# Kernel optimization log

Hardware: AMD Instinct MI355X
Metric: run time of the kernel (lower is better)

Reference implementation:

```python
import jax, jax.numpy as jnp
import numpy as np

NUM_SLOTS = 2048
LATENT_DIM = 512
EPS = 1e-12  # torch F.normalize clamps norm at eps


def _l2_normalize(x, axis):
    n = jnp.linalg.norm(x, axis=axis, keepdims=True)
    return x / jnp.maximum(n, EPS)


def setup_inputs() -> dict:
    key = jax.random.key(0)
    k_z, k_m = jax.random.split(key)
    z = jax.random.normal(k_z, (65536, LATENT_DIM), dtype=jnp.float32)
    memory = jax.random.normal(k_m, (NUM_SLOTS, LATENT_DIM), dtype=jnp.float32)
    return {"z": z, "memory": memory}


def reference(z, memory):
    # cosine-similarity attention over memory slots
    z_norm = _l2_normalize(z, axis=1)          # [B, D]
    mem_norm = _l2_normalize(memory, axis=1)   # [N, D]
    attn = jax.nn.softmax(z_norm @ mem_norm.T, axis=1)  # [B, N]
    z_hat = attn @ memory                      # [B, D] (unnormalized memory, as in source)
    return (z_hat, attn)
```

## Files before the change

kernel.cpp:

```cpp
#include <hip/hip_runtime.h>

#define NSLOTS 2048
#define DIM    512

typedef __bf16 bf16x8 __attribute__((ext_vector_type(8)));
typedef float  f32x4  __attribute__((ext_vector_type(4)));
typedef unsigned short us4 __attribute__((ext_vector_type(4)));
typedef unsigned short us8 __attribute__((ext_vector_type(8)));

typedef const __attribute__((address_space(1))) unsigned* gp_t;
typedef __attribute__((address_space(3))) unsigned* sp_t;

__device__ __forceinline__ void gl16(const void* g, void* l) {
    __builtin_amdgcn_global_load_lds((gp_t)g, (sp_t)l, 16, 0, 0);
}

__device__ __forceinline__ unsigned short f2bf(float f) {
    unsigned u = __builtin_bit_cast(unsigned, f);
    u = (u + 0x7FFFu + ((u >> 16) & 1u)) >> 16;
    return (unsigned short)u;
}
__device__ __forceinline__ float bf2f(unsigned short u) {
    unsigned v = ((unsigned)u) << 16;
    return __builtin_bit_cast(float, v);
}

__global__ __launch_bounds__(512) void prep_kernel(const float* __restrict__ mem,
                                                   unsigned short* __restrict__ memN,
                                                   unsigned short* __restrict__ memT) {
    __shared__ unsigned short T[32][516];
    const int tid = threadIdx.x;
    const int sl  = tid >> 4;
    const int c16 = tid & 15;
    const int n   = blockIdx.x * 32 + sl;
    const f32x4* row = (const f32x4*)(mem + (size_t)n * DIM);
    f32x4 v[8];
    float s = 0.f;
    #pragma unroll
    for (int j = 0; j < 8; ++j) {
        v[j] = row[c16*8 + j];
        s += v[j][0]*v[j][0] + v[j][1]*v[j][1] + v[j][2]*v[j][2] + v[j][3]*v[j][3];
    }
    #pragma unroll
    for (int off = 1; off < 16; off <<= 1) s += __shfl_xor(s, off);
    const float rn = 1.0f / fmaxf(sqrtf(s), 1e-12f);
    #pragma unroll
    for (int j = 0; j < 8; ++j) {
        us4 p, q;
        #pragma unroll
        for (int e = 0; e < 4; ++e) { p[e] = f2bf(v[j][e] * rn); q[e] = f2bf(v[j][e]); }
        *(us4*)(memN + (size_t)n * DIM + c16*32 + j*4) = p;
        *(us4*)(&T[sl][c16*32 + j*4]) = q;
    }
    __syncthreads();
    {
        const int d = tid;
        const int c4 = tid & 3;
        #pragma unroll
        for (int i = 0; i < 4; ++i) {
            const int dd = i*128 + (tid >> 2);
            us8 g;
            #pragma unroll
            for (int j = 0; j < 8; ++j) g[j] = T[c4*8 + j][dd];
            *(us8*)(memT + (size_t)dd * NSLOTS + blockIdx.x*32 + c4*8) = g;
        }
        (void)d;
    }
}

__global__ __launch_bounds__(512) void zprep_kernel(const float* __restrict__ z,
                                                    float* attnB) {
    const int tid = threadIdx.x;
    const size_t row = (size_t)blockIdx.x * 64 + (tid >> 3);
    const int c8 = tid & 7;
    const f32x4* zr = (const f32x4*)(z + row * DIM);
    f32x4 v[16];
    float s = 0.f;
    #pragma unroll
    for (int j = 0; j < 16; ++j) {
        v[j] = __builtin_nontemporal_load(zr + c8 + j*8);
        s += v[j][0]*v[j][0] + v[j][1]*v[j][1] + v[j][2]*v[j][2] + v[j][3]*v[j][3];
    }
    s += __shfl_xor(s, 1); s += __shfl_xor(s, 2); s += __shfl_xor(s, 4);
    const float rn = 1.0f / fmaxf(sqrtf(s), 1e-12f);
    char* dst = (char*)attnB + row * 8192 + 3072;
    #pragma unroll
    for (int j = 0; j < 16; ++j) {
        us4 p;
        #pragma unroll
        for (int e = 0; e < 4; ++e) p[e] = f2bf(v[j][e] * rn);
        *(us4*)(dst + c8*8 + j*64) = p;
    }
}

__global__ __launch_bounds__(512, 4) void k1_kernel(const unsigned short* __restrict__ memN,
                                                    float* attnB,
                                                    float* __restrict__ sums) {
    __shared__ char sb[2][24576];
    __shared__ float wsums[4][64];
    const int tid  = threadIdx.x;
    const int wid  = tid >> 6;
    const int lane = tid & 63;
    const int l16  = lane & 15;
    const int l4   = lane >> 4;
    const int m    = wid >> 2, n = wid & 3;
    const size_t rowbase = (size_t)blockIdx.x * 64;
    const char* attnRd = (const char*)attnB;

    auto stage = [&](int buf, int t) {
        const int c = t >> 3, ks = t & 7;
        {
            const int f = wid*64 + lane, ar = f >> 3, g = f & 7;
            const char* src = attnRd + (rowbase + ar) * 8192 + 3072 + ks*128
                            + ((g*16) ^ ((ar & 7) << 4));
            gl16(src, &sb[buf][0] + wid*1024);
        }
        #pragma unroll
        for (int i = 0; i < 2; ++i) {
            const int f = (i*8 + wid)*64 + lane, br = f >> 3, g = f & 7;
            const char* src = (const char*)memN + (size_t)(c*128 + br) * 1024 + ks*128
                            + ((g*16) ^ ((br & 7) << 4));
            gl16(src, &sb[buf][8192] + (i*8 + wid)*1024);
        }
    };

    const f32x4 zeroV = {0.f, 0.f, 0.f, 0.f};
    f32x4 acc[2][2];
    #pragma unroll
    for (int mt = 0; mt < 2; ++mt)
        #pragma unroll
        for (int nt = 0; nt < 2; ++nt) acc[mt][nt] = zeroV;
    float psum[2][4];
    #pragma unroll
    for (int mt = 0; mt < 2; ++mt)
        #pragma unroll
        for (int r = 0; r < 4; ++r) psum[mt][r] = 0.f;

    stage(0, 0);
    __syncthreads();

    for (int t = 0; t < 128; ++t) {
        const int c = t >> 3, ks = t & 7;
        if (t < 127) stage((t + 1) & 1, t + 1);
        const char* Ab = (const char*)&sb[t & 1][0];
        const char* Bb = (const char*)&sb[t & 1][8192];
        #pragma unroll
        for (int kk = 0; kk < 2; ++kk) {
            bf16x8 af[2];
            #pragma unroll
            for (int mt = 0; mt < 2; ++mt) {
                const int ar = m*32 + mt*16 + l16;
                af[mt] = *(const bf16x8*)(Ab + ar*128 + ((kk*64 + l4*16) ^ ((ar & 7) << 4)));
            }
            #pragma unroll
            for (int nt = 0; nt < 2; ++nt) {
                const int br = n*32 + nt*16 + l16;
                bf16x8 b = *(const bf16x8*)(Bb + br*128 + ((kk*64 + l4*16) ^ ((br & 7) << 4)));
                acc[0][nt] = __builtin_amdgcn_mfma_f32_16x16x32_bf16(af[0], b, acc[0][nt], 0, 0, 0);
                acc[1][nt] = __builtin_amdgcn_mfma_f32_16x16x32_bf16(af[1], b, acc[1][nt], 0, 0, 0);
            }
        }
        __syncthreads();
        if (ks == 7) {
            char* Pl = (char*)&sb[t & 1][0];
            #pragma unroll
            for (int mt = 0; mt < 2; ++mt)
                #pragma unroll
                for (int nt = 0; nt < 2; ++nt)
                    #pragma unroll
                    for (int r = 0; r < 4; ++r) {
                        const float e = __expf(acc[mt][nt][r]);
                        psum[mt][r] += e;
                        const int row = m*32 + mt*16 + l4*4 + r;
                        const int sl  = n*32 + nt*16 + l16;
                        *(unsigned short*)(Pl + row*256 + (((sl >> 3) * 16) ^ ((row & 7) << 4)) + (sl & 7)*2) = f2bf(e);
                        acc[mt][nt][r] = 0.f;
                    }
            __syncthreads();
            {
                const int prow = tid >> 3;
                #pragma unroll
                for (int h = 0; h < 2; ++h) {
                    const int g = (tid & 7) + h*8;
                    us8 pv = *(const us8*)(Pl + prow*256 + ((g*16) ^ ((prow & 7) << 4)));
                    __builtin_nontemporal_store(pv,
                        (us8*)((char*)attnB + (rowbase + prow) * 8192 + 4096 + c*256 + g*16));
                }
            }
            __syncthreads();
        }
    }

    #pragma unroll
    for (int mt = 0; mt < 2; ++mt)
        #pragma unroll
        for (int r = 0; r < 4; ++r) {
            #pragma unroll
            for (int off = 1; off < 16; off <<= 1) psum[mt][r] += __shfl_xor(psum[mt][r], off);
        }
    if (l16 == 0) {
        #pragma unroll
        for (int mt = 0; mt < 2; ++mt)
            #pragma unroll
            for (int r = 0; r < 4; ++r)
                wsums[n][m*32 + mt*16 + l4*4 + r] = psum[mt][r];
    }
    __syncthreads();
    if (tid < 64) sums[rowbase + tid] = wsums[0][tid] + wsums[1][tid] + wsums[2][tid] + wsums[3][tid];
}

__global__ __launch_bounds__(512, 4) void k2_kernel(const unsigned short* __restrict__ memT,
                                                    const float* __restrict__ sums,
                                                    float* __restrict__ zhat,
                                                    float* attnB) {
    __shared__ char ab[2][8192];
    __shared__ char bb[2][16384];
    __shared__ float rsums[64];
    const int tid  = threadIdx.x;
    const int wid  = tid >> 6;
    const int lane = tid & 63;
    const int l16  = lane & 15;
    const int l4   = lane >> 4;
    const int m    = wid >> 2, n = wid & 3;
    const size_t rowbase = (size_t)blockIdx.x * 64;
    const char* attnRd = (const char*)attnB;

    auto stageA = [&](int buf, int ks) {
        const int f = wid*64 + lane, ar = f >> 3, g = f & 7;
        const char* src = attnRd + (rowbase + ar) * 8192 + 4096 + ks*128
                        + ((g*16) ^ ((ar & 7) << 4));
        gl16(src, &ab[buf][0] + wid*1024);
    };
    auto stageB = [&](int buf, int ks, int nb) {
        #pragma unroll
        for (int i = 0; i < 2; ++i) {
            const int f = (i*8 + wid)*64 + lane, dr = f >> 3, g = f & 7;
            const char* src = (const char*)memT + (size_t)(nb*128 + dr) * 4096 + ks*128
                            + ((g*16) ^ ((dr & 7) << 4));
            gl16(src, &bb[buf][0] + (i*8 + wid)*1024);
        }
    };

    if (tid < 64) rsums[tid] = 1.0f / sums[rowbase + tid];

    const f32x4 zeroV = {0.f, 0.f, 0.f, 0.f};
    f32x4 acc[4][2][2];
    #pragma unroll
    for (int nb = 0; nb < 4; ++nb)
        #pragma unroll
        for (int mt = 0; mt < 2; ++mt)
            #pragma unroll
            for (int nt = 0; nt < 2; ++nt) acc[nb][mt][nt] = zeroV;

    stageA(0, 0);
    stageB(0, 0, 0);
    __syncthreads();

    for (int ks = 0; ks < 32; ++ks) {
        #pragma unroll
        for (int nb = 0; nb < 4; ++nb) {
            const int u = ks*4 + nb;
            if (nb < 3) stageB((u + 1) & 1, ks, nb + 1);
            else if (ks < 31) { stageA((ks + 1) & 1, ks + 1); stageB((u + 1) & 1, ks + 1, 0); }
            const char* Ab = (const char*)&ab[ks & 1][0];
            const char* Bb = (const char*)&bb[u & 1][0];
            if (nb == 0) {
                const int prow = tid >> 3;
                const int g = tid & 7;
                const float sc = rsums[prow];
                us8 pv = *(const us8*)(Ab + prow*128 + ((g*16) ^ ((prow & 7) << 4)));
                f32x4 o0, o1;
                #pragma unroll
                for (int e = 0; e < 4; ++e) { o0[e] = bf2f(pv[e]) * sc; o1[e] = bf2f(pv[e + 4]) * sc; }
                float* dst = attnB + (rowbase + prow) * NSLOTS + ks*64 + g*8;
                __builtin_nontemporal_store(o0, (f32x4*)dst);
                __builtin_nontemporal_store(o1, (f32x4*)(dst + 4));
            }
            #pragma unroll
            for (int kk = 0; kk < 2; ++kk) {
                bf16x8 af[2];
                #pragma unroll
                for (int mt = 0; mt < 2; ++mt) {
                    const int ar = m*32 + mt*16 + l16;
                    af[mt] = *(const bf16x8*)(Ab + ar*128 + ((kk*64 + l4*16) ^ ((ar & 7) << 4)));
                }
                #pragma unroll
                for (int nt = 0; nt < 2; ++nt) {
                    const int dr = n*32 + nt*16 + l16;
                    bf16x8 b = *(const bf16x8*)(Bb + dr*128 + ((kk*64 + l4*16) ^ ((dr & 7) << 4)));
                    acc[nb][0][nt] = __builtin_amdgcn_mfma_f32_16x16x32_bf16(af[0], b, acc[nb][0][nt], 0, 0, 0);
                    acc[nb][1][nt] = __builtin_amdgcn_mfma_f32_16x16x32_bf16(af[1], b, acc[nb][1][nt], 0, 0, 0);
                }
            }
            __syncthreads();
        }
    }

    #pragma unroll
    for (int nb = 0; nb < 4; ++nb)
        #pragma unroll
        for (int mt = 0; mt < 2; ++mt)
            #pragma unroll
            for (int r = 0; r < 4; ++r) {
                const int row = m*32 + mt*16 + l4*4 + r;
                const float rs = rsums[row];
                float* zr = zhat + (rowbase + row) * DIM + nb*128 + n*32 + l16;
                __builtin_nontemporal_store(acc[nb][mt][0][r] * rs, zr);
                __builtin_nontemporal_store(acc[nb][mt][1][r] * rs, zr + 16);
            }
}

extern "C" void kernel_launch(void* const* d_in, const int* in_sizes, int n_in,
                              void* d_out, int out_size, void* d_ws, size_t ws_size,
                              hipStream_t stream) {
    const float* zin = (const float*)d_in[0];
    const float* mem = (const float*)d_in[1];
    const int B = in_sizes[0] / DIM;
    unsigned short* memN = (unsigned short*)d_ws;
    unsigned short* memT = memN + (size_t)NSLOTS * DIM;
    float* sums = (float*)(memT + (size_t)NSLOTS * DIM);
    float* zhat = (float*)d_out;
    float* attn = zhat + (size_t)B * DIM;
    prep_kernel<<<NSLOTS / 32, 512, 0, stream>>>(mem, memN, memT);
    zprep_kernel<<<B / 64, 512, 0, stream>>>(zin, attn);
    k1_kernel<<<B / 64, 512, 0, stream>>>(memN, attn, sums);
    k2_kernel<<<B / 64, 512, 0, stream>>>(memT, sums, zhat, attn);
}
```

Baseline: 554.1 us.

## Fuse z normalization into k1, keep A resident in LDS, widen tiles

The separate zprep kernel is removed. k1 now normalizes z rows itself and keeps the full 64x512 bf16 A tile resident in LDS, so A no longer round-trips through global memory. k1's slot tile per chunk doubles to 256, and k2's K-step doubles to 256 bytes per row. In exchange, LDS use per block grows sharply (about 128KB in k1 and 96KB in k2) and the minimum-occupancy hint is dropped, which cuts the number of resident blocks per CU.

```diff
diff --git a/kernel.cpp b/kernel.cpp
--- a/kernel.cpp
+++ b/kernel.cpp
@@ -54,7 +54,6 @@
     }
     __syncthreads();
     {
-        const int d = tid;
         const int c4 = tid & 3;
         #pragma unroll
         for (int i = 0; i < 4; ++i) {
@@ -64,39 +63,15 @@
             for (int j = 0; j < 8; ++j) g[j] = T[c4*8 + j][dd];
             *(us8*)(memT + (size_t)dd * NSLOTS + blockIdx.x*32 + c4*8) = g;
         }
-        (void)d;
-    }
-}
-
-__global__ __launch_bounds__(512) void zprep_kernel(const float* __restrict__ z,
-                                                    float* attnB) {
-    const int tid = threadIdx.x;
-    const size_t row = (size_t)blockIdx.x * 64 + (tid >> 3);
-    const int c8 = tid & 7;
-    const f32x4* zr = (const f32x4*)(z + row * DIM);
-    f32x4 v[16];
-    float s = 0.f;
-    #pragma unroll
-    for (int j = 0; j < 16; ++j) {
-        v[j] = __builtin_nontemporal_load(zr + c8 + j*8);
-        s += v[j][0]*v[j][0] + v[j][1]*v[j][1] + v[j][2]*v[j][2] + v[j][3]*v[j][3];
-    }
-    s += __shfl_xor(s, 1); s += __shfl_xor(s, 2); s += __shfl_xor(s, 4);
-    const float rn = 1.0f / fmaxf(sqrtf(s), 1e-12f);
-    char* dst = (char*)attnB + row * 8192 + 3072;
-    #pragma unroll
-    for (int j = 0; j < 16; ++j) {
-        us4 p;
-        #pragma unroll
-        for (int e = 0; e < 4; ++e) p[e] = f2bf(v[j][e] * rn);
-        *(us4*)(dst + c8*8 + j*64) = p;
-    }
-}
-
-__global__ __launch_bounds__(512, 4) void k1_kernel(const unsigned short* __restrict__ memN,
-                                                    float* attnB,
-                                                    float* __restrict__ sums) {
-    __shared__ char sb[2][24576];
+    }
+}
+
+__global__ __launch_bounds__(512) void k1_kernel(const float* __restrict__ z,
+                                                 const unsigned short* __restrict__ memN,
+                                                 float* attnB,
+                                                 float* __restrict__ sums) {
+    __shared__ char As[65536];
+    __shared__ char Bs[2][32768];
     __shared__ float wsums[4][64];
     const int tid  = threadIdx.x;
     const int wid  = tid >> 6;
@@ -105,56 +80,70 @@
     const int l4   = lane >> 4;
     const int m    = wid >> 2, n = wid & 3;
     const size_t rowbase = (size_t)blockIdx.x * 64;
-    const char* attnRd = (const char*)attnB;
-
-    auto stage = [&](int buf, int t) {
+
+    {
+        const int r = tid >> 3, c8 = tid & 7;
+        const f32x4* zr = (const f32x4*)(z + (rowbase + r) * DIM);
+        f32x4 v[16];
+        float s = 0.f;
+        #pragma unroll
+        for (int j = 0; j < 16; ++j) {
+            v[j] = __builtin_nontemporal_load(zr + c8 + j*8);
+            s += v[j][0]*v[j][0] + v[j][1]*v[j][1] + v[j][2]*v[j][2] + v[j][3]*v[j][3];
+        }
+        s += __shfl_xor(s, 1); s += __shfl_xor(s, 2); s += __shfl_xor(s, 4);
+        const float rn = 1.0f / fmaxf(sqrtf(s), 1e-12f);
+        char* arow = As + r*1024;
+        #pragma unroll
+        for (int j = 0; j < 16; ++j) {
+            us4 p;
+            #pragma unroll
+            for (int e = 0; e < 4; ++e) p[e] = f2bf(v[j][e] * rn);
+            *(us4*)(arow + ((c8*8 + j*64) ^ ((r & 7) << 4))) = p;
+        }
+    }
+
+    auto stageB = [&](int buf, int t) {
         const int c = t >> 3, ks = t & 7;
-        {
-            const int f = wid*64 + lane, ar = f >> 3, g = f & 7;
-            const char* src = attnRd + (rowbase + ar) * 8192 + 3072 + ks*128
-                            + ((g*16) ^ ((ar & 7) << 4));
-            gl16(src, &sb[buf][0] + wid*1024);
-        }
-        #pragma unroll
-        for (int i = 0; i < 2; ++i) {
+        #pragma unroll
+        for (int i = 0; i < 4; ++i) {
             const int f = (i*8 + wid)*64 + lane, br = f >> 3, g = f & 7;
-            const char* src = (const char*)memN + (size_t)(c*128 + br) * 1024 + ks*128
+            const char* src = (const char*)memN + (size_t)(c*256 + br) * 1024 + ks*128
                             + ((g*16) ^ ((br & 7) << 4));
-            gl16(src, &sb[buf][8192] + (i*8 + wid)*1024);
+            gl16(src, &Bs[buf][(i*8 + wid)*1024]);
         }
     };
 
     const f32x4 zeroV = {0.f, 0.f, 0.f, 0.f};
-    f32x4 acc[2][2];
+    f32x4 acc[2][4];
     #pragma unroll
     for (int mt = 0; mt < 2; ++mt)
         #pragma unroll
-        for (int nt = 0; nt < 2; ++nt) acc[mt][nt] = zeroV;
+        for (int nt = 0; nt < 4; ++nt) acc[mt][nt] = zeroV;
     float psum[2][4];
     #pragma unroll
     for (int mt = 0; mt < 2; ++mt)
         #pragma unroll
         for (int r = 0; r < 4; ++r) psum[mt][r] = 0.f;
 
-    stage(0, 0);
+    stageB(0, 0);
     __syncthreads();
 
-    for (int t = 0; t < 128; ++t) {
+    for (int t = 0; t < 64; ++t) {
         const int c = t >> 3, ks = t & 7;
-        if (t < 127) stage((t + 1) & 1, t + 1);
-        const char* Ab = (const char*)&sb[t & 1][0];
-        const char* Bb = (const char*)&sb[t & 1][8192];
+        if (t < 63) stageB((t + 1) & 1, t + 1);
+        const char* Bb = (const char*)&Bs[t & 1][0];
         #pragma unroll
         for (int kk = 0; kk < 2; ++kk) {
             bf16x8 af[2];
             #pragma unroll
             for (int mt = 0; mt < 2; ++mt) {
                 const int ar = m*32 + mt*16 + l16;
-                af[mt] = *(const bf16x8*)(Ab + ar*128 + ((kk*64 + l4*16) ^ ((ar & 7) << 4)));
-            }
-            #pragma unroll
-            for (int nt = 0; nt < 2; ++nt) {
-                const int br = n*32 + nt*16 + l16;
+                af[mt] = *(const bf16x8*)(As + ar*1024 + ((ks*128 + kk*64 + l4*16) ^ ((ar & 7) << 4)));
+            }
+            #pragma unroll
+            for (int nt = 0; nt < 4; ++nt) {
+                const int br = n*64 + nt*16 + l16;
                 bf16x8 b = *(const bf16x8*)(Bb + br*128 + ((kk*64 + l4*16) ^ ((br & 7) << 4)));
                 acc[0][nt] = __builtin_amdgcn_mfma_f32_16x16x32_bf16(af[0], b, acc[0][nt], 0, 0, 0);
                 acc[1][nt] = __builtin_amdgcn_mfma_f32_16x16x32_bf16(af[1], b, acc[1][nt], 0, 0, 0);
@@ -162,29 +151,28 @@
         }
         __syncthreads();
         if (ks == 7) {
-            char* Pl = (char*)&sb[t & 1][0];
+            char* Pl = (char*)&Bs[t & 1][0];
             #pragma unroll
             for (int mt = 0; mt < 2; ++mt)
                 #pragma unroll
-                for (int nt = 0; nt < 2; ++nt)
+                for (int nt = 0; nt < 4; ++nt)
                     #pragma unroll
                     for (int r = 0; r < 4; ++r) {
                         const float e = __expf(acc[mt][nt][r]);
                         psum[mt][r] += e;
                         const int row = m*32 + mt*16 + l4*4 + r;
-                        const int sl  = n*32 + nt*16 + l16;
-                        *(unsigned short*)(Pl + row*256 + (((sl >> 3) * 16) ^ ((row & 7) << 4)) + (sl & 7)*2) = f2bf(e);
+                        const int sl  = n*64 + nt*16 + l16;
+                        *(unsigned short*)(Pl + row*512 + (((sl >> 3) * 16) ^ ((row & 7) << 4)) + (sl & 7)*2) = f2bf(e);
                         acc[mt][nt][r] = 0.f;
                     }
             __syncthreads();
             {
-                const int prow = tid >> 3;
-                #pragma unroll
-                for (int h = 0; h < 2; ++h) {
-                    const int g = (tid & 7) + h*8;
-                    us8 pv = *(const us8*)(Pl + prow*256 + ((g*16) ^ ((prow & 7) << 4)));
-                    __builtin_nontemporal_store(pv,
-                        (us8*)((char*)attnB + (rowbase + prow) * 8192 + 4096 + c*256 + g*16));
+                const int prow = tid >> 3, g8 = tid & 7;
+                char* gdst = (char*)attnB + (rowbase + prow) * 8192 + 4096 + c*512;
+                #pragma unroll
+                for (int h = 0; h < 4; ++h) {
+                    us8 pv = *(const us8*)(Pl + prow*512 + (((g8 + h*8)*16) ^ ((prow & 7) << 4)));
+                    __builtin_nontemporal_store(pv, (us8*)(gdst + (g8 + h*8)*16));
                 }
             }
             __syncthreads();
@@ -209,12 +197,12 @@
     if (tid < 64) sums[rowbase + tid] = wsums[0][tid] + wsums[1][tid] + wsums[2][tid] + wsums[3][tid];
 }
 
-__global__ __launch_bounds__(512, 4) void k2_kernel(const unsigned short* __restrict__ memT,
-                                                    const float* __restrict__ sums,
-                                                    float* __restrict__ zhat,
-                                                    float* attnB) {
-    __shared__ char ab[2][8192];
-    __shared__ char bb[2][16384];
+__global__ __launch_bounds__(512) void k2_kernel(const unsigned short* __restrict__ memT,
+                                                 const float* __restrict__ sums,
+                                                 float* __restrict__ zhat,
+                                                 float* attnB) {
+    __shared__ char ab[2][16384];
+    __shared__ char bb[2][32768];
     __shared__ float rsums[64];
     const int tid  = threadIdx.x;
     const int wid  = tid >> 6;
@@ -225,19 +213,22 @@
     const size_t rowbase = (size_t)blockIdx.x * 64;
     const char* attnRd = (const char*)attnB;
 
-    auto stageA = [&](int buf, int ks) {
-        const int f = wid*64 + lane, ar = f >> 3, g = f & 7;
-        const char* src = attnRd + (rowbase + ar) * 8192 + 4096 + ks*128
-                        + ((g*16) ^ ((ar & 7) << 4));
-        gl16(src, &ab[buf][0] + wid*1024);
+    auto stageA = [&](int buf, int ks2) {
+        #pragma unroll
+        for (int i = 0; i < 2; ++i) {
+            const int f = (i*8 + wid)*64 + lane, ar = f >> 4, g = f & 15;
+            const char* src = attnRd + (rowbase + ar) * 8192 + 4096 + ks2*256
+                            + ((g*16) ^ ((ar & 7) << 4));
+            gl16(src, &ab[buf][(i*8 + wid)*1024]);
+        }
     };
-    auto stageB = [&](int buf, int ks, int nb) {
-        #pragma unroll
-        for (int i = 0; i < 2; ++i) {
-            const int f = (i*8 + wid)*64 + lane, dr = f >> 3, g = f & 7;
-            const char* src = (const char*)memT + (size_t)(nb*128 + dr) * 4096 + ks*128
+    auto stageB = [&](int buf, int ks2, int nb) {
+        #pragma unroll
+        for (int i = 0; i < 4; ++i) {
+            const int f = (i*8 + wid)*64 + lane, dr = f >> 4, g = f & 15;
+            const char* src = (const char*)memT + (size_t)(nb*128 + dr) * 4096 + ks2*256
                             + ((g*16) ^ ((dr & 7) << 4));
-            gl16(src, &bb[buf][0] + (i*8 + wid)*1024);
+            gl16(src, &bb[buf][(i*8 + wid)*1024]);
         }
     };
 
@@ -256,38 +247,40 @@
     stageB(0, 0, 0);
     __syncthreads();
 
-    for (int ks = 0; ks < 32; ++ks) {
+    for (int ks2 = 0; ks2 < 16; ++ks2) {
         #pragma unroll
         for (int nb = 0; nb < 4; ++nb) {
-            const int u = ks*4 + nb;
-            if (nb < 3) stageB((u + 1) & 1, ks, nb + 1);
-            else if (ks < 31) { stageA((ks + 1) & 1, ks + 1); stageB((u + 1) & 1, ks + 1, 0); }
-            const char* Ab = (const char*)&ab[ks & 1][0];
+            const int u = ks2*4 + nb;
+            if (nb < 3) stageB((u + 1) & 1, ks2, nb + 1);
+            else if (ks2 < 15) { stageA((ks2 + 1) & 1, ks2 + 1); stageB((u + 1) & 1, ks2 + 1, 0); }
+            const char* Ab = (const char*)&ab[ks2 & 1][0];
             const char* Bb = (const char*)&bb[u & 1][0];
             if (nb == 0) {
-                const int prow = tid >> 3;
-                const int g = tid & 7;
+                const int prow = tid >> 3, g8 = tid & 7;
                 const float sc = rsums[prow];
-                us8 pv = *(const us8*)(Ab + prow*128 + ((g*16) ^ ((prow & 7) << 4)));
-                f32x4 o0, o1;
-                #pragma unroll
-                for (int e = 0; e < 4; ++e) { o0[e] = bf2f(pv[e]) * sc; o1[e] = bf2f(pv[e + 4]) * sc; }
-                float* dst = attnB + (rowbase + prow) * NSLOTS + ks*64 + g*8;
-                __builtin_nontemporal_store(o0, (f32x4*)dst);
-                __builtin_nontemporal_store(o1, (f32x4*)(dst + 4));
-            }
-            #pragma unroll
-            for (int kk = 0; kk < 2; ++kk) {
+                float* dst = attnB + (rowbase + prow) * NSLOTS + ks2*128 + g8*8;
+                #pragma unroll
+                for (int h = 0; h < 2; ++h) {
+                    us8 pv = *(const us8*)(Ab + prow*256 + (((g8 + h*8)*16) ^ ((prow & 7) << 4)));
+                    f32x4 o0, o1;
+                    #pragma unroll
+                    for (int e = 0; e < 4; ++e) { o0[e] = bf2f(pv[e]) * sc; o1[e] = bf2f(pv[e + 4]) * sc; }
+                    __builtin_nontemporal_store(o0, (f32x4*)(dst + h*64));
+                    __builtin_nontemporal_store(o1, (f32x4*)(dst + h*64 + 4));
+                }
+            }
+            #pragma unroll
+            for (int kk = 0; kk < 4; ++kk) {
                 bf16x8 af[2];
                 #pragma unroll
                 for (int mt = 0; mt < 2; ++mt) {
                     const int ar = m*32 + mt*16 + l16;
-                    af[mt] = *(const bf16x8*)(Ab + ar*128 + ((kk*64 + l4*16) ^ ((ar & 7) << 4)));
+                    af[mt] = *(const bf16x8*)(Ab + ar*256 + ((kk*64 + l4*16) ^ ((ar & 7) << 4)));
                 }
                 #pragma unroll
                 for (int nt = 0; nt < 2; ++nt) {
                     const int dr = n*32 + nt*16 + l16;
-                    bf16x8 b = *(const bf16x8*)(Bb + dr*128 + ((kk*64 + l4*16) ^ ((dr & 7) << 4)));
+                    bf16x8 b = *(const bf16x8*)(Bb + dr*256 + ((kk*64 + l4*16) ^ ((dr & 7) << 4)));
                     acc[nb][0][nt] = __builtin_amdgcn_mfma_f32_16x16x32_bf16(af[0], b, acc[nb][0][nt], 0, 0, 0);
                     acc[nb][1][nt] = __builtin_amdgcn_mfma_f32_16x16x32_bf16(af[1], b, acc[nb][1][nt], 0, 0, 0);
                 }
@@ -322,7 +315,6 @@
     float* zhat = (float*)d_out;
     float* attn = zhat + (size_t)B * DIM;
     prep_kernel<<<NSLOTS / 32, 512, 0, stream>>>(mem, memN, memT);
-    zprep_kernel<<<B / 64, 512, 0, stream>>>(zin, attn);
-    k1_kernel<<<B / 64, 512, 0, stream>>>(memN, attn, sums);
+    k1_kernel<<<B / 64, 512, 0, stream>>>(zin, memN, attn, sums);
     k2_kernel<<<B / 64, 512, 0, stream>>>(memT, sums, zhat, attn);
 }
```

Result: slower. 676.6 us (+22.1%).

## Fuse z normalization into k1, keeping normalized z in registers

Applied to the files above, without the earlier changes.

Removes the separate zprep kernel, which wrote bf16-normalized z into scratch space in the attn output buffer, and moves that work into k1. Each k1 thread now loads its z row segment, normalizes it, and holds the bf16 result in registers, writing it into LDS every k-step instead of re-reading it from global memory each chunk. This drops one kernel launch and the global round trip of normalized z. In exchange it adds register pressure (8 us8 per thread), removes the occupancy hint of 4 from launch_bounds, and splits LDS into separate A and B buffers.

```diff
diff --git a/kernel.cpp b/kernel.cpp
--- a/kernel.cpp
+++ b/kernel.cpp
@@ -54,7 +54,6 @@
     }
     __syncthreads();
     {
-        const int d = tid;
         const int c4 = tid & 3;
         #pragma unroll
         for (int i = 0; i < 4; ++i) {
@@ -64,39 +63,15 @@
             for (int j = 0; j < 8; ++j) g[j] = T[c4*8 + j][dd];
             *(us8*)(memT + (size_t)dd * NSLOTS + blockIdx.x*32 + c4*8) = g;
         }
-        (void)d;
-    }
-}
-
-__global__ __launch_bounds__(512) void zprep_kernel(const float* __restrict__ z,
-                                                    float* attnB) {
-    const int tid = threadIdx.x;
-    const size_t row = (size_t)blockIdx.x * 64 + (tid >> 3);
-    const int c8 = tid & 7;
-    const f32x4* zr = (const f32x4*)(z + row * DIM);
-    f32x4 v[16];
-    float s = 0.f;
-    #pragma unroll
-    for (int j = 0; j < 16; ++j) {
-        v[j] = __builtin_nontemporal_load(zr + c8 + j*8);
-        s += v[j][0]*v[j][0] + v[j][1]*v[j][1] + v[j][2]*v[j][2] + v[j][3]*v[j][3];
-    }
-    s += __shfl_xor(s, 1); s += __shfl_xor(s, 2); s += __shfl_xor(s, 4);
-    const float rn = 1.0f / fmaxf(sqrtf(s), 1e-12f);
-    char* dst = (char*)attnB + row * 8192 + 3072;
-    #pragma unroll
-    for (int j = 0; j < 16; ++j) {
-        us4 p;
-        #pragma unroll
-        for (int e = 0; e < 4; ++e) p[e] = f2bf(v[j][e] * rn);
-        *(us4*)(dst + c8*8 + j*64) = p;
-    }
-}
-
-__global__ __launch_bounds__(512, 4) void k1_kernel(const unsigned short* __restrict__ memN,
-                                                    float* attnB,
-                                                    float* __restrict__ sums) {
-    __shared__ char sb[2][24576];
+    }
+}
+
+__global__ __launch_bounds__(512) void k1_kernel(const float* __restrict__ z,
+                                                 const unsigned short* __restrict__ memN,
+                                                 float* attnB,
+                                                 float* __restrict__ sums) {
+    __shared__ char As[2][8192];
+    __shared__ char Bs[2][16384];
     __shared__ float wsums[4][64];
     const int tid  = threadIdx.x;
     const int wid  = tid >> 6;
@@ -105,22 +80,41 @@
     const int l4   = lane >> 4;
     const int m    = wid >> 2, n = wid & 3;
     const size_t rowbase = (size_t)blockIdx.x * 64;
-    const char* attnRd = (const char*)attnB;
-
-    auto stage = [&](int buf, int t) {
+    const int r  = tid >> 3;
+    const int c8 = tid & 7;
+    const int aoff = r*128 + ((c8*16) ^ ((r & 7) << 4));
+
+    us8 a[8];
+    {
+        const f32x4* zr = (const f32x4*)(z + (rowbase + r) * DIM);
+        f32x4 va[8], vb[8];
+        float s = 0.f;
+        #pragma unroll
+        for (int j = 0; j < 8; ++j) {
+            va[j] = __builtin_nontemporal_load(zr + c8*2 + j*16);
+            vb[j] = __builtin_nontemporal_load(zr + c8*2 + 1 + j*16);
+            s += va[j][0]*va[j][0] + va[j][1]*va[j][1] + va[j][2]*va[j][2] + va[j][3]*va[j][3]
+               + vb[j][0]*vb[j][0] + vb[j][1]*vb[j][1] + vb[j][2]*vb[j][2] + vb[j][3]*vb[j][3];
+        }
+        s += __shfl_xor(s, 1); s += __shfl_xor(s, 2); s += __shfl_xor(s, 4);
+        const float rn = 1.0f / fmaxf(sqrtf(s), 1e-12f);
+        #pragma unroll
+        for (int j = 0; j < 8; ++j) {
+            us8 p;
+            #pragma unroll
+            for (int e = 0; e < 4; ++e) { p[e] = f2bf(va[j][e] * rn); p[e + 4] = f2bf(vb[j][e] * rn); }
+            a[j] = p;
+        }
+    }
+
+    auto stageB = [&](int buf, int t) {
         const int c = t >> 3, ks = t & 7;
-        {
-            const int f = wid*64 + lane, ar = f >> 3, g = f & 7;
-            const char* src = attnRd + (rowbase + ar) * 8192 + 3072 + ks*128
-                            + ((g*16) ^ ((ar & 7) << 4));
-            gl16(src, &sb[buf][0] + wid*1024);
-        }
         #pragma unroll
         for (int i = 0; i < 2; ++i) {
             const int f = (i*8 + wid)*64 + lane, br = f >> 3, g = f & 7;
             const char* src = (const char*)memN + (size_t)(c*128 + br) * 1024 + ks*128
                             + ((g*16) ^ ((br & 7) << 4));
-            gl16(src, &sb[buf][8192] + (i*8 + wid)*1024);
+            gl16(src, &Bs[buf][(i*8 + wid)*1024]);
         }
     };
 
@@ -134,76 +128,82 @@
     #pragma unroll
     for (int mt = 0; mt < 2; ++mt)
         #pragma unroll
-        for (int r = 0; r < 4; ++r) psum[mt][r] = 0.f;
-
-    stage(0, 0);
+        for (int rr = 0; rr < 4; ++rr) psum[mt][rr] = 0.f;
+
+    *(us8*)(&As[0][aoff]) = a[0];
+    stageB(0, 0);
     __syncthreads();
 
-    for (int t = 0; t < 128; ++t) {
-        const int c = t >> 3, ks = t & 7;
-        if (t < 127) stage((t + 1) & 1, t + 1);
-        const char* Ab = (const char*)&sb[t & 1][0];
-        const char* Bb = (const char*)&sb[t & 1][8192];
-        #pragma unroll
-        for (int kk = 0; kk < 2; ++kk) {
-            bf16x8 af[2];
-            #pragma unroll
-            for (int mt = 0; mt < 2; ++mt) {
-                const int ar = m*32 + mt*16 + l16;
-                af[mt] = *(const bf16x8*)(Ab + ar*128 + ((kk*64 + l4*16) ^ ((ar & 7) << 4)));
-            }
-            #pragma unroll
-            for (int nt = 0; nt < 2; ++nt) {
-                const int br = n*32 + nt*16 + l16;
-                bf16x8 b = *(const bf16x8*)(Bb + br*128 + ((kk*64 + l4*16) ^ ((br & 7) << 4)));
-                acc[0][nt] = __builtin_amdgcn_mfma_f32_16x16x32_bf16(af[0], b, acc[0][nt], 0, 0, 0);
-                acc[1][nt] = __builtin_amdgcn_mfma_f32_16x16x32_bf16(af[1], b, acc[1][nt], 0, 0, 0);
-            }
-        }
-        __syncthreads();
-        if (ks == 7) {
-            char* Pl = (char*)&sb[t & 1][0];
-            #pragma unroll
-            for (int mt = 0; mt < 2; ++mt)
-                #pragma unroll
-                for (int nt = 0; nt < 2; ++nt)
+    for (int c = 0; c < 16; ++c) {
+        #pragma unroll
+        for (int ks = 0; ks < 8; ++ks) {
+            const int t = c*8 + ks;
+            if (t < 127) {
+                *(us8*)(&As[(t + 1) & 1][aoff]) = a[(ks + 1) & 7];
+                stageB((t + 1) & 1, t + 1);
+            }
+            const char* Ab = (const char*)As[t & 1];
+            const char* Bb = (const char*)Bs[t & 1];
+            #pragma unroll
+            for (int kk = 0; kk < 2; ++kk) {
+                bf16x8 af[2];
+                #pragma unroll
+                for (int mt = 0; mt < 2; ++mt) {
+                    const int ar = m*32 + mt*16 + l16;
+                    af[mt] = *(const bf16x8*)(Ab + ar*128 + ((kk*64 + l4*16) ^ ((ar & 7) << 4)));
+                }
+                #pragma unroll
+                for (int nt = 0; nt < 2; ++nt) {
+                    const int br = n*32 + nt*16 + l16;
+                    bf16x8 b = *(const bf16x8*)(Bb + br*128 + ((kk*64 + l4*16) ^ ((br & 7) << 4)));
+                    acc[0][nt] = __builtin_amdgcn_mfma_f32_16x16x32_bf16(af[0], b, acc[0][nt], 0, 0, 0);
+                    acc[1][nt] = __builtin_amdgcn_mfma_f32_16x16x32_bf16(af[1], b, acc[1][nt], 0, 0, 0);
+                }
+            }
+            __syncthreads();
+            if (ks == 7) {
+                char* Pl = (char*)Bs[t & 1];
+                #pragma unroll
+                for (int mt = 0; mt < 2; ++mt)
                     #pragma unroll
-                    for (int r = 0; r < 4; ++r) {
-                        const float e = __expf(acc[mt][nt][r]);
-                        psum[mt][r] += e;
-                        const int row = m*32 + mt*16 + l4*4 + r;
-                        const int sl  = n*32 + nt*16 + l16;
-                        *(unsigned short*)(Pl + row*256 + (((sl >> 3) * 16) ^ ((row & 7) << 4)) + (sl & 7)*2) = f2bf(e);
-                        acc[mt][nt][r] = 0.f;
+                    for (int nt = 0; nt < 2; ++nt)
+                        #pragma unroll
+                        for (int rr = 0; rr < 4; ++rr) {
+                            const float e = __expf(acc[mt][nt][rr]);
+                            psum[mt][rr] += e;
+                            const int row = m*32 + mt*16 + l4*4 + rr;
+                            const int sl  = n*32 + nt*16 + l16;
+                            *(unsigned short*)(Pl + row*256 + (((sl >> 3) * 16) ^ ((row & 7) << 4)) + (sl & 7)*2) = f2bf(e);
+                            acc[mt][nt][rr] = 0.f;
+                        }
+                __syncthreads();
+                {
+                    const int prow = tid >> 3, g8 = tid & 7;
+                    char* gdst = (char*)attnB + (rowbase + prow) * 8192 + 4096 + c*256;
+                    #pragma unroll
+                    for (int h = 0; h < 2; ++h) {
+                        us8 pv = *(const us8*)(Pl + prow*256 + (((g8 + h*8)*16) ^ ((prow & 7) << 4)));
+                        __builtin_nontemporal_store(pv, (us8*)(gdst + (g8 + h*8)*16));
                     }
-            __syncthreads();
-            {
-                const int prow = tid >> 3;
-                #pragma unroll
-                for (int h = 0; h < 2; ++h) {
-                    const int g = (tid & 7) + h*8;
-                    us8 pv = *(const us8*)(Pl + prow*256 + ((g*16) ^ ((prow & 7) << 4)));
-                    __builtin_nontemporal_store(pv,
-                        (us8*)((char*)attnB + (rowbase + prow) * 8192 + 4096 + c*256 + g*16));
-                }
-            }
-            __syncthreads();
+                }
+                __syncthreads();
+            }
         }
     }
 
     #pragma unroll
     for (int mt = 0; mt < 2; ++mt)
         #pragma unroll
-        for (int r = 0; r < 4; ++r) {
-            #pragma unroll
-            for (int off = 1; off < 16; off <<= 1) psum[mt][r] += __shfl_xor(psum[mt][r], off);
+        for (int rr = 0; rr < 4; ++rr) {
+            #pragma unroll
+            for (int off = 1; off < 16; off <<= 1) psum[mt][rr] += __shfl_xor(psum[mt][rr], off);
         }
     if (l16 == 0) {
         #pragma unroll
         for (int mt = 0; mt < 2; ++mt)
             #pragma unroll
-            for (int r = 0; r < 4; ++r)
-                wsums[n][m*32 + mt*16 + l4*4 + r] = psum[mt][r];
+            for (int rr = 0; rr < 4; ++rr)
+                wsums[n][m*32 + mt*16 + l4*4 + rr] = psum[mt][rr];
     }
     __syncthreads();
     if (tid < 64) sums[rowbase + tid] = wsums[0][tid] + wsums[1][tid] + wsums[2][tid] + wsums[3][tid];
@@ -301,12 +301,12 @@
         #pragma unroll
         for (int mt = 0; mt < 2; ++mt)
             #pragma unroll
-            for (int r = 0; r < 4; ++r) {
-                const int row = m*32 + mt*16 + l4*4 + r;
+            for (int rr = 0; rr < 4; ++rr) {
+                const int row = m*32 + mt*16 + l4*4 + rr;
                 const float rs = rsums[row];
                 float* zr = zhat + (rowbase + row) * DIM + nb*128 + n*32 + l16;
-                __builtin_nontemporal_store(acc[nb][mt][0][r] * rs, zr);
-                __builtin_nontemporal_store(acc[nb][mt][1][r] * rs, zr + 16);
+                __builtin_nontemporal_store(acc[nb][mt][0][rr] * rs, zr);
+                __builtin_nontemporal_store(acc[nb][mt][1][rr] * rs, zr + 16);
             }
 }
 
@@ -322,7 +322,6 @@
     float* zhat = (float*)d_out;
     float* attn = zhat + (size_t)B * DIM;
     prep_kernel<<<NSLOTS / 32, 512, 0, stream>>>(mem, memN, memT);
-    zprep_kernel<<<B / 64, 512, 0, stream>>>(zin, attn);
-    k1_kernel<<<B / 64, 512, 0, stream>>>(memN, attn, sums);
+    k1_kernel<<<B / 64, 512, 0, stream>>>(zin, memN, attn, sums);
     k2_kernel<<<B / 64, 512, 0, stream>>>(memT, sums, zhat, attn);
 }
```

Result: faster. 490.9 us (-11.4%).
